# Optimization experiments

Measured on AMD Instinct MI355X. Metric: run time of the kernel, lower is better.

The kernel has to match this reference:

```python
import jax, jax.numpy as jnp
import numpy as np

EPS_BN = 1e-5
EPS_NORM = 1e-12
NUM_HEADS = 8


def _bn_relu(x):
    # BatchNorm2d in training mode with fresh params (gamma=1, beta=0), then ReLU.
    m = x.mean((0, 2, 3), keepdims=True)
    v = x.var((0, 2, 3), keepdims=True)  # biased variance, as PyTorch uses for normalization
    return jax.nn.relu((x - m) * jax.lax.rsqrt(v + EPS_BN))


def _conv3(x, w, groups=1):
    # 3x3 conv, stride 1, padding 1 (NCHW / OIHW)
    return jax.lax.conv_general_dilated(
        x, w, (1, 1), ((1, 1), (1, 1)),
        dimension_numbers=('NCHW', 'OIHW', 'NCHW'),
        feature_group_count=groups)


def _encoder(x, w1, w2, w3):
    # Conv1x1 -> BN -> ReLU -> Conv k2 s2 -> BN -> ReLU -> Conv1x1 -> BN -> ReLU
    x = _bn_relu(jnp.einsum('bihw,oi->bohw', x, w1))
    b, c, h, w = x.shape
    # k=2,s=2 conv as a reshape + einsum (non-overlapping 2x2 patches)
    x = _bn_relu(jnp.einsum('bchpwq,ocpq->bohw', x.reshape(b, c, h // 2, 2, w // 2, 2), w2))
    return _bn_relu(jnp.einsum('bihw,oi->bohw', x, w3))


def _decoder(x, w1, w2, w3):
    # ConvT1x1 -> BN -> ReLU -> ConvT k2 s2 -> BN -> ReLU -> ConvT1x1 -> BN -> ReLU
    x = _bn_relu(jnp.einsum('bihw,io->bohw', x, w1))
    # ConvTranspose k=2,s=2: each input pixel expands to a 2x2 block
    y = jnp.einsum('bihw,iopq->bohpwq', x, w2)
    b, o, h, p, w, q = y.shape
    x = _bn_relu(y.reshape(b, o, h * p, w * q))
    return _bn_relu(jnp.einsum('bihw,io->bohw', x, w3))


def _l2norm(x):
    # F.normalize(dim=-1) with eps=1e-12
    return x / jnp.maximum(jnp.linalg.norm(x, axis=-1, keepdims=True), EPS_NORM)


def setup_inputs() -> dict:
    key = jax.random.key(0)
    ks = jax.random.split(key, 13)
    B, C, H, W = 8, 256, 64, 64
    d = C // 4  # attention dim after self.divide

    def rn(k, shape, s=0.1):
        return jax.random.normal(k, shape, jnp.float32) * s

    return {
        'x': jax.random.normal(ks[0], (B, C, H, W), jnp.float32),
        'y': jax.random.normal(ks[1], (B, C, H, W), jnp.float32),
        'temperature': jnp.ones((NUM_HEADS, 1, 1), jnp.float32),
        'enc_w1': rn(ks[2], (d // 2, C)),
        'enc_w2': rn(ks[3], (d // 2, d // 2, 2, 2)),
        'enc_w3': rn(ks[4], (d, d // 2)),
        'kv_w': rn(ks[5], (2 * d, d)),
        'kv_dw_w': rn(ks[6], (2 * d, 1, 3, 3)),
        'q_w': rn(ks[7], (d, d)),
        'q_dw_w': rn(ks[8], (d, d, 3, 3)),
        'proj_w': rn(ks[9], (d, d)),
        'dec_w1': rn(ks[10], (d, 2 * d)),
        'dec_w2': rn(ks[11], (2 * d, 2 * d, 2, 2)),
        'dec_w3': rn(ks[12], (2 * d, 4 * d)),
    }


def reference(x, y, temperature, enc_w1, enc_w2, enc_w3, kv_w, kv_dw_w,
              q_w, q_dw_w, proj_w, dec_w1, dec_w2, dec_w3):
    # Shared freshly-built encoder applied to both x and y (same weights,
    # BN batch stats computed per call).
    x = _encoder(x, enc_w1, enc_w2, enc_w3)
    y = _encoder(y, enc_w1, enc_w2, enc_w3)
    b, c, h, w = x.shape  # c = 64, h = w = 32

    kv = _conv3(jnp.einsum('bihw,oi->bohw', x, kv_w), kv_dw_w, groups=2 * c)
    k, v = jnp.split(kv, 2, axis=1)
    q = _conv3(jnp.einsum('bihw,oi->bohw', y, q_w), q_dw_w)  # regular 3x3 conv

    ch = c // NUM_HEADS
    heads = lambda t: t.reshape(b, NUM_HEADS, ch, h * w)  # b head c (h w)
    q, k, v = heads(q), heads(k), heads(v)
    q = _l2norm(q)
    k = _l2norm(k)
    temp = temperature[None]  # [1, head, 1, 1]

    # Spatial attention: [b, head, hw, hw]
    attn_s = jax.nn.softmax(jnp.einsum('bhcn,bhcm->bhnm', q, k) * temp, axis=-1)
    out_s = jnp.einsum('bhcn,bhnm->bhcm', v, attn_s).reshape(b, c, h, w)
    out_s = jnp.einsum('bihw,oi->bohw', out_s, proj_w)

    # Channel attention: [b, head, c, c]
    attn_c = jax.nn.softmax(jnp.einsum('bhcn,bhdn->bhcd', q, k) * temp, axis=-1)
    out_c = jnp.einsum('bhcd,bhdn->bhcn', attn_c, v).reshape(b, c, h, w)
    out_c = jnp.einsum('bihw,oi->bohw', out_c, proj_w)

    return _decoder(out_s + out_c, dec_w1, dec_w2, dec_w3)
```

## Files before the change

### kernel.cpp

```cpp
#include <hip/hip_runtime.h>
#include <hip/hip_bf16.h>

#define EPS_BN 1e-5f

#define PIPE_FENCE() asm volatile("" ::: "memory")

template<int OT, bool HASBN, bool HASSTATS>
__global__ __launch_bounds__(256,2) void conv1x1_lds(
    const float* __restrict__ in0, const float* __restrict__ in1,
    const float* __restrict__ w, float* __restrict__ out,
    const float* __restrict__ stIn, float* __restrict__ stOut,
    int I, int O, int P, int wio, int zsplit, float invN)
{
  constexpr int OB = 4*OT;
  __shared__ __align__(16) float wl[8192];
  __shared__ __align__(16) float4 il[2][8][64];
  __shared__ float bnm[256], bnr[256];

  int tid = threadIdx.x;
  int c   = tid & 63;
  int g   = tid >> 6;
  int z = blockIdx.z;
  int t = (z >= zsplit) ? 1 : 0;
  int b = t ? (z - zsplit) : z;
  const float* in = t ? in1 : in0;
  int o0 = blockIdx.y*OB;
  int P4 = P >> 2;

  if(wio){
    for(int idx=tid; idx<I*OB; idx+=256){
      int i = idx/OB, oo = idx - i*OB;
      wl[idx] = w[(size_t)i*O + o0 + oo];
    }
  } else {
    for(int idx=tid; idx<I*OB; idx+=256){
      int oo = idx/I, i = idx - oo*I;
      wl[i*OB + oo] = w[(size_t)(o0+oo)*I + i];
    }
  }
  if(HASBN){
    for(int i=tid; i<I; i+=256){
      float s  = stIn[((size_t)t*I + i)*2];
      float s2 = stIn[((size_t)t*I + i)*2+1];
      float m  = s*invN;
      bnm[i] = m;
      bnr[i] = rsqrtf(s2*invN - m*m + EPS_BN);
    }
  }

  const float4* inb = (const float4*)(in + (size_t)b*I*P) + (size_t)blockIdx.x*64;

  float4 vr0 = inb[(size_t)g*P4 + c];
  float4 vr1 = inb[(size_t)(g+4)*P4 + c];
  il[0][g][c]   = vr0;
  il[0][g+4][c] = vr1;
  __syncthreads();

  float acc[OT][4];
#pragma unroll
  for(int j=0;j<OT;j++){ acc[j][0]=acc[j][1]=acc[j][2]=acc[j][3]=0.f; }

  int nchunk = I >> 3;
  for(int k=0; k<nchunk; ++k){
    int cur = k & 1;
    if(k+1 < nchunk){
      vr0 = inb[(size_t)((k+1)*8+g)*P4 + c];
      vr1 = inb[(size_t)((k+1)*8+g+4)*P4 + c];
    }
    PIPE_FENCE();
#pragma unroll
    for(int ch=0; ch<8; ++ch){
      float4 v = il[cur][ch][c];
      if(HASBN){
        int i = k*8+ch;
        float m = bnm[i], r = bnr[i];
        v.x = fmaxf((v.x-m)*r, 0.f); v.y = fmaxf((v.y-m)*r, 0.f);
        v.z = fmaxf((v.z-m)*r, 0.f); v.w = fmaxf((v.w-m)*r, 0.f);
      }
      const float4* wr4 = (const float4*)&wl[(k*8+ch)*OB + g*OT];
#pragma unroll
      for(int j4=0;j4<OT/4;j4++){
        float4 wq = wr4[j4];
        int j = j4*4;
        acc[j  ][0]=fmaf(wq.x,v.x,acc[j  ][0]); acc[j  ][1]=fmaf(wq.x,v.y,acc[j  ][1]);
        acc[j  ][2]=fmaf(wq.x,v.z,acc[j  ][2]); acc[j  ][3]=fmaf(wq.x,v.w,acc[j  ][3]);
        acc[j+1][0]=fmaf(wq.y,v.x,acc[j+1][0]); acc[j+1][1]=fmaf(wq.y,v.y,acc[j+1][1]);
        acc[j+1][2]=fmaf(wq.y,v.z,acc[j+1][2]); acc[j+1][3]=fmaf(wq.y,v.w,acc[j+1][3]);
        acc[j+2][0]=fmaf(wq.z,v.x,acc[j+2][0]); acc[j+2][1]=fmaf(wq.z,v.y,acc[j+2][1]);
        acc[j+2][2]=fmaf(wq.z,v.z,acc[j+2][2]); acc[j+2][3]=fmaf(wq.z,v.w,acc[j+2][3]);
        acc[j+3][0]=fmaf(wq.w,v.x,acc[j+3][0]); acc[j+3][1]=fmaf(wq.w,v.y,acc[j+3][1]);
        acc[j+3][2]=fmaf(wq.w,v.z,acc[j+3][2]); acc[j+3][3]=fmaf(wq.w,v.w,acc[j+3][3]);
      }
    }
    PIPE_FENCE();
    if(k+1 < nchunk){
      int nxt = cur^1;
      il[nxt][g][c]   = vr0;
      il[nxt][g+4][c] = vr1;
    }
    __syncthreads();
  }

  float4* ob = (float4*)(out + (size_t)z*O*P) + (size_t)blockIdx.x*64 + c;
#pragma unroll
  for(int j=0;j<OT;j++){
    float4 vv = {acc[j][0], acc[j][1], acc[j][2], acc[j][3]};
    ob[(size_t)(o0 + g*OT + j)*P4] = vv;
  }

  if(HASSTATS){
#pragma unroll
    for(int j=0;j<OT;j++){
      float s  = acc[j][0]+acc[j][1]+acc[j][2]+acc[j][3];
      float s2 = acc[j][0]*acc[j][0]+acc[j][1]*acc[j][1]
               + acc[j][2]*acc[j][2]+acc[j][3]*acc[j][3];
      for(int off=32; off>0; off>>=1){
        s  += __shfl_down(s,  off, 64);
        s2 += __shfl_down(s2, off, 64);
      }
      if((tid & 63)==0){
        atomicAdd(&stOut[((size_t)t*O + o0 + g*OT + j)*2],   s);
        atomicAdd(&stOut[((size_t)t*O + o0 + g*OT + j)*2+1], s2);
      }
    }
  }
}

template<int OT, bool HASBN, bool HASSTATS>
__global__ __launch_bounds__(256) void conv1x1_small(
    const float* __restrict__ in0, const float* __restrict__ in1,
    const float* __restrict__ w, float* __restrict__ out,
    const float* __restrict__ stIn, float* __restrict__ stOut,
    int I, int O, int wio, int zsplit, float invN)
{
  __shared__ float wl[512];
  __shared__ float bnm[128], bnr[128];
  int tid = threadIdx.x;
  int z  = blockIdx.z;
  int t  = (z >= zsplit) ? 1 : 0;
  int b  = t ? (z - zsplit) : z;
  const float* in = t ? in1 : in0;
  int W2 = 2*OT;

  for(int idx=tid; idx<I*W2; idx+=256){
    int i = idx/W2, slot = idx - i*W2;
    int oabs = blockIdx.y*W2 + slot;
    wl[idx] = wio ? w[(size_t)i*O + oabs] : w[(size_t)oabs*I + i];
  }
  if(HASBN){
    for(int i=tid; i<I; i+=256){
      float s  = stIn[((size_t)t*I + i)*2];
      float s2 = stIn[((size_t)t*I + i)*2+1];
      float m  = s*invN;
      bnm[i] = m;
      bnr[i] = rsqrtf(s2*invN - m*m + EPS_BN);
    }
  }
  __syncthreads();

  int p4 = blockIdx.x*128 + (tid & 127);
  int os = tid >> 7;
  const float4* inb = (const float4*)(in + (size_t)b*I*1024) + p4;

  float acc[OT][4];
#pragma unroll
  for(int j=0;j<OT;j++){ acc[j][0]=acc[j][1]=acc[j][2]=acc[j][3]=0.f; }

  float4 vb[8];
  for(int i0=0;i0<I;i0+=8){
#pragma unroll
    for(int u=0;u<8;u++) vb[u] = inb[(size_t)(i0+u)*256];
    PIPE_FENCE();
#pragma unroll
    for(int u=0;u<8;u++){
      float4 v = vb[u];
      if(HASBN){
        float m = bnm[i0+u], r = bnr[i0+u];
        v.x = fmaxf((v.x-m)*r, 0.f); v.y = fmaxf((v.y-m)*r, 0.f);
        v.z = fmaxf((v.z-m)*r, 0.f); v.w = fmaxf((v.w-m)*r, 0.f);
      }
      const float* wr = &wl[(i0+u)*W2 + os*OT];
#pragma unroll
      for(int j=0;j<OT;j++){
        float wv = wr[j];
        acc[j][0] = fmaf(wv, v.x, acc[j][0]);
        acc[j][1] = fmaf(wv, v.y, acc[j][1]);
        acc[j][2] = fmaf(wv, v.z, acc[j][2]);
        acc[j][3] = fmaf(wv, v.w, acc[j][3]);
      }
    }
  }

  int obase = blockIdx.y*W2 + os*OT;
  float4* ob = (float4*)(out + ((size_t)z*O + obase)*1024) + p4;
#pragma unroll
  for(int j=0;j<OT;j++){
    float4 vv = {acc[j][0], acc[j][1], acc[j][2], acc[j][3]};
    ob[(size_t)j*256] = vv;
  }

  if(HASSTATS){
#pragma unroll
    for(int j=0;j<OT;j++){
      float s  = acc[j][0]+acc[j][1]+acc[j][2]+acc[j][3];
      float s2 = acc[j][0]*acc[j][0]+acc[j][1]*acc[j][1]
               + acc[j][2]*acc[j][2]+acc[j][3]*acc[j][3];
      for(int off=32; off>0; off>>=1){
        s  += __shfl_down(s,  off, 64);
        s2 += __shfl_down(s2, off, 64);
      }
      if((tid & 63)==0){
        atomicAdd(&stOut[((size_t)t*O + obase + j)*2],   s);
        atomicAdd(&stOut[((size_t)t*O + obase + j)*2+1], s2);
      }
    }
  }
}

__global__ __launch_bounds__(256) void conv2x2s2_bn_kernel(
    const float* __restrict__ in, const float* __restrict__ w,
    float* __restrict__ out, const float* __restrict__ stIn,
    float* __restrict__ stOut, float invN)
{
  __shared__ float wl[512];
  __shared__ float bnm[32], bnr[32];
  int tid = threadIdx.x;
  int o0 = blockIdx.x*4;
  int rq = blockIdx.y;
  int z  = blockIdx.z;
  int t  = z >> 3;

  for(int idx=tid; idx<512; idx+=256){
    int osub = idx>>7, ch=(idx>>2)&31, pq=idx&3;
    wl[idx] = w[(((size_t)(o0+osub)*32 + ch)*4) + pq];
  }
  if(tid < 32){
    float s  = stIn[((size_t)t*32 + tid)*2];
    float s2 = stIn[((size_t)t*32 + tid)*2+1];
    float m  = s*invN;
    bnm[tid] = m;
    bnr[tid] = rsqrtf(s2*invN - m*m + EPS_BN);
  }
  __syncthreads();

  int os   = tid >> 6;
  int slot = tid & 63;
  int h    = rq*8 + (slot>>3);
  int wg   = slot & 7;
  int cb   = wg*8;
  const float* wbase = &wl[os*128];
  const float* inz = in + (size_t)z*32*4096;

  float acc[4] = {0,0,0,0};
  float4 c0,c1,c2,c3, n0_,n1_,n2_,n3_;
  c0 = *(const float4*)(inz + (size_t)0*4096 + (2*h)*64 + cb);
  c1 = *(const float4*)(inz + (size_t)0*4096 + (2*h)*64 + cb + 4);
  c2 = *(const float4*)(inz + (size_t)0*4096 + (2*h+1)*64 + cb);
  c3 = *(const float4*)(inz + (size_t)0*4096 + (2*h+1)*64 + cb + 4);
  for(int ch=0; ch<32; ch++){
    if(ch < 31){
      n0_ = *(const float4*)(inz + (size_t)(ch+1)*4096 + (2*h)*64 + cb);
      n1_ = *(const float4*)(inz + (size_t)(ch+1)*4096 + (2*h)*64 + cb + 4);
      n2_ = *(const float4*)(inz + (size_t)(ch+1)*4096 + (2*h+1)*64 + cb);
      n3_ = *(const float4*)(inz + (size_t)(ch+1)*4096 + (2*h+1)*64 + cb + 4);
    }
    float m = bnm[ch], r = bnr[ch];
    float t0[8] = {c0.x,c0.y,c0.z,c0.w,c1.x,c1.y,c1.z,c1.w};
    float t1[8] = {c2.x,c2.y,c2.z,c2.w,c3.x,c3.y,c3.z,c3.w};
#pragma unroll
    for(int e=0;e<8;e++){
      t0[e] = fmaxf((t0[e]-m)*r, 0.f);
      t1[e] = fmaxf((t1[e]-m)*r, 0.f);
    }
    const float* wp = wbase + ch*4;
#pragma unroll
    for(int k=0;k<4;k++){
      acc[k] = fmaf(wp[0], t0[2*k],   acc[k]);
      acc[k] = fmaf(wp[1], t0[2*k+1], acc[k]);
      acc[k] = fmaf(wp[2], t1[2*k],   acc[k]);
      acc[k] = fmaf(wp[3], t1[2*k+1], acc[k]);
    }
    c0=n0_; c1=n1_; c2=n2_; c3=n3_;
  }

  float4 vv = {acc[0],acc[1],acc[2],acc[3]};
  *(float4*)(out + ((size_t)z*32 + o0+os)*1024 + h*32 + wg*4) = vv;

  float s  = acc[0]+acc[1]+acc[2]+acc[3];
  float s2 = acc[0]*acc[0]+acc[1]*acc[1]+acc[2]*acc[2]+acc[3]*acc[3];
  for(int off=32; off>0; off>>=1){
    s  += __shfl_down(s,  off, 64);
    s2 += __shfl_down(s2, off, 64);
  }
  if((tid & 63)==0){
    atomicAdd(&stOut[((size_t)t*32 + o0 + os)*2],   s);
    atomicAdd(&stOut[((size_t)t*32 + o0 + os)*2+1], s2);
  }
}

__global__ __launch_bounds__(256) void upsample2x2_bn_kernel(
    const float* __restrict__ in, const float* __restrict__ w,
    float* __restrict__ out, const float* __restrict__ stIn,
    float* __restrict__ stOut, float invN)
{
  __shared__ float wl[1024];
  __shared__ float bnm[128], bnr[128];
  int tid = threadIdx.x;
  int o0 = blockIdx.x*2;
  int b  = blockIdx.y;

  for(int idx=tid; idx<1024; idx+=256){
    int pq = idx & 3, r = idx >> 2;
    int i = r >> 1, j = r & 1;
    wl[idx] = w[((size_t)i*128 + o0+j)*4 + pq];
  }
  if(tid < 128){
    float s  = stIn[(size_t)tid*2];
    float s2 = stIn[(size_t)tid*2+1];
    float m  = s*invN;
    bnm[tid] = m;
    bnr[tid] = rsqrtf(s2*invN - m*m + EPS_BN);
  }
  __syncthreads();

  int h  = tid >> 3;
  int wg = tid & 7;
  int w0 = wg*4;

  float acc[2][16];
#pragma unroll
  for(int j=0;j<2;j++) for(int e=0;e<16;e++) acc[j][e]=0.f;

  float4 vb4[8];
  for(int i0=0;i0<128;i0+=8){
#pragma unroll
    for(int u=0;u<8;u++)
      vb4[u] = *(const float4*)(in + (((size_t)b*128+i0+u)*1024) + h*32 + w0);
    PIPE_FENCE();
#pragma unroll
    for(int u=0;u<8;u++){
      int i = i0+u;
      float4 v = vb4[u];
      float m = bnm[i], r = bnr[i];
      float vk[4] = {fmaxf((v.x-m)*r,0.f), fmaxf((v.y-m)*r,0.f),
                     fmaxf((v.z-m)*r,0.f), fmaxf((v.w-m)*r,0.f)};
#pragma unroll
      for(int j=0;j<2;j++){
        const float* wj = &wl[(i*2+j)*4];
#pragma unroll
        for(int pq=0;pq<4;pq++){
#pragma unroll
          for(int k=0;k<4;k++)
            acc[j][pq*4+k] = fmaf(wj[pq], vk[k], acc[j][pq*4+k]);
        }
      }
    }
  }

#pragma unroll
  for(int j=0;j<2;j++){
    float* ob = out + ((size_t)b*128 + o0+j)*4096;
#pragma unroll
    for(int p=0;p<2;p++){
      float4 A = {acc[j][(p*2+0)*4+0], acc[j][(p*2+1)*4+0],
                  acc[j][(p*2+0)*4+1], acc[j][(p*2+1)*4+1]};
      float4 B = {acc[j][(p*2+0)*4+2], acc[j][(p*2+1)*4+2],
                  acc[j][(p*2+0)*4+3], acc[j][(p*2+1)*4+3]};
      *(float4*)(ob + (2*h+p)*64 + 2*w0)     = A;
      *(float4*)(ob + (2*h+p)*64 + 2*w0 + 4) = B;
    }
  }

#pragma unroll
  for(int j=0;j<2;j++){
    float s=0.f, s2=0.f;
#pragma unroll
    for(int e=0;e<16;e++){ s += acc[j][e]; s2 += acc[j][e]*acc[j][e]; }
    for(int off=32; off>0; off>>=1){
      s  += __shfl_down(s,  off, 64);
      s2 += __shfl_down(s2, off, 64);
    }
    if((tid & 63)==0){
      atomicAdd(&stOut[((size_t)(o0+j))*2],   s);
      atomicAdd(&stOut[((size_t)(o0+j))*2+1], s2);
    }
  }
}

__global__ __launch_bounds__(256) void bn_final_kernel(
    float* __restrict__ x, const float* __restrict__ st, float invN)
{
  int idx4 = blockIdx.x*256 + threadIdx.x;
  int c = (idx4 >> 10) & 255;
  float s  = st[(size_t)c*2];
  float s2 = st[(size_t)c*2+1];
  float m  = s*invN;
  float r  = rsqrtf(s2*invN - m*m + EPS_BN);
  float4 v = ((float4*)x)[idx4];
  v.x = fmaxf((v.x-m)*r, 0.f); v.y = fmaxf((v.y-m)*r, 0.f);
  v.z = fmaxf((v.z-m)*r, 0.f); v.w = fmaxf((v.w-m)*r, 0.f);
  ((float4*)x)[idx4] = v;
}

__global__ __launch_bounds__(256) void dwconv3x3_kernel(
    const float* __restrict__ in, const float* __restrict__ w,
    float* __restrict__ out, int C)
{
  int c = blockIdx.x, b = blockIdx.y;
  int tid = threadIdx.x;
  __shared__ float wl[9];
  if(tid < 9) wl[tid] = w[c*9 + tid];
  __syncthreads();
  int h = tid >> 3, x4 = tid & 7;
  int c0 = x4*4;
  const float* base = in + ((size_t)b*C + c)*1024;
  float ax=0.f, ay=0.f, az=0.f, aw=0.f;
#pragma unroll
  for(int dr=0; dr<3; dr++){
    int r = h + dr - 1;
    if((unsigned)r >= 32u) continue;
    const float* row = base + r*32 + c0;
    float4 cc = *(const float4*)row;
    float l  = (x4>0) ? row[-1] : 0.f;
    float rr = (x4<7) ? row[4]  : 0.f;
    float w0=wl[dr*3], w1=wl[dr*3+1], w2=wl[dr*3+2];
    ax = fmaf(w0,l,   fmaf(w1,cc.x, fmaf(w2,cc.y, ax)));
    ay = fmaf(w0,cc.x,fmaf(w1,cc.y, fmaf(w2,cc.z, ay)));
    az = fmaf(w0,cc.y,fmaf(w1,cc.z, fmaf(w2,cc.w, az)));
    aw = fmaf(w0,cc.z,fmaf(w1,cc.w, fmaf(w2,rr,  aw)));
  }
  float4 vv = {ax,ay,az,aw};
  *(float4*)(out + ((size_t)b*C + c)*1024 + h*32 + c0) = vv;
}

__global__ __launch_bounds__(256) void conv3x3_kernel(
    const float* __restrict__ in, const float* __restrict__ w,
    float* __restrict__ out, int IC)
{
  int o = blockIdx.x, b = blockIdx.y;
  int tid = threadIdx.x;
  __shared__ float wl[576];
  for(int t=tid; t<IC*9; t+=256) wl[t] = w[(size_t)o*IC*9 + t];
  __syncthreads();
  int h = tid >> 3, x4 = tid & 7;
  int c0 = x4*4;
  const float* inb = in + (size_t)b*IC*1024;
  float ax=0.f, ay=0.f, az=0.f, aw=0.f;
#pragma unroll 2
  for(int i=0;i<IC;i++){
    const float* base = inb + (size_t)i*1024;
    const float* wp = &wl[i*9];
#pragma unroll
    for(int dr=0; dr<3; dr++){
      int r = h + dr - 1;
      if((unsigned)r >= 32u) continue;
      const float* row = base + r*32 + c0;
      float4 cc = *(const float4*)row;
      float l  = (x4>0) ? row[-1] : 0.f;
      float rr = (x4<7) ? row[4]  : 0.f;
      float w0=wp[dr*3], w1=wp[dr*3+1], w2=wp[dr*3+2];
      ax = fmaf(w0,l,   fmaf(w1,cc.x, fmaf(w2,cc.y, ax)));
      ay = fmaf(w0,cc.x,fmaf(w1,cc.y, fmaf(w2,cc.z, ay)));
      az = fmaf(w0,cc.y,fmaf(w1,cc.z, fmaf(w2,cc.w, az)));
      aw = fmaf(w0,cc.z,fmaf(w1,cc.w, fmaf(w2,rr,  aw)));
    }
  }
  float4 vv = {ax,ay,az,aw};
  *(float4*)(out + ((size_t)b*gridDim.x + o)*1024 + h*32 + c0) = vv;
}

__global__ __launch_bounds__(256) void norm_scale_kernel(
    const float* __restrict__ q, const float* __restrict__ kv,
    float* __restrict__ scl)
{
  int r = blockIdx.x;
  const float* p;
  if(r < 512){ int b=r>>6, c=r&63; p = q + ((size_t)b*64+c)*1024; }
  else { int rr=r-512; int b=rr>>6, c=rr&63; p = kv + ((size_t)b*128+c)*1024; }
  int tid = threadIdx.x;
  float4 v = ((const float4*)p)[tid];
  float s = v.x*v.x + v.y*v.y + v.z*v.z + v.w*v.w;
  __shared__ float ls[256];
  ls[tid]=s; __syncthreads();
  for(int st=128; st>0; st>>=1){ if(tid<st) ls[tid]+=ls[tid+st]; __syncthreads(); }
  if(tid==0) scl[r] = 1.f/fmaxf(sqrtf(ls[0]), 1e-12f);
}

__global__ __launch_bounds__(256) void attn_pass1(
    const float* __restrict__ q, const float* __restrict__ kv,
    const float* __restrict__ temp, const float* __restrict__ scl,
    float* __restrict__ den_out)
{
  int bx = blockIdx.x, hh = blockIdx.y, b = blockIdx.z;
  int nchunk = bx >> 2, mq = bx & 3;
  int tid = threadIdx.x;
  __shared__ __align__(16) float kl[256*12];
  const float* kb = kv + ((size_t)b*128 + hh*8)*1024 + mq*256;
  for(int t=tid;t<2048;t+=256){
    int c=t>>8, m=t&255;
    kl[m*12+c] = kb[(size_t)c*1024+m] * scl[512 + b*64 + hh*8 + c];
  }
  __syncthreads();
  int n = nchunk*256 + tid;
  const float* qp = q + ((size_t)b*64 + hh*8)*1024 + n;
  float th = temp[hh];
  float mxb = fabsf(th);
  float qr[8];
#pragma unroll
  for(int c=0;c<8;c++) qr[c] = qp[(size_t)c*1024] * scl[b*64+hh*8+c] * th;
  const float4* kl4 = (const float4*)kl;
  float den = 0.f, den2 = 0.f;
  for(int m=0;m<256;m+=2){
    float4 a  = kl4[m*3],     a2 = kl4[m*3+1];
    float4 bt = kl4[(m+1)*3], b2 = kl4[(m+1)*3+1];
    float s0 = qr[0]*a.x+qr[1]*a.y+qr[2]*a.z+qr[3]*a.w
             + qr[4]*a2.x+qr[5]*a2.y+qr[6]*a2.z+qr[7]*a2.w;
    float s1 = qr[0]*bt.x+qr[1]*bt.y+qr[2]*bt.z+qr[3]*bt.w
             + qr[4]*b2.x+qr[5]*b2.y+qr[6]*b2.z+qr[7]*b2.w;
    den  += __expf(s0 - mxb);
    den2 += __expf(s1 - mxb);
  }
  atomicAdd(&den_out[((size_t)(b*8+hh))*1024+n], den+den2);
}

__global__ __launch_bounds__(256) void attn_pass2(
    const float* __restrict__ q, const float* __restrict__ kv,
    const float* __restrict__ temp, const float* __restrict__ scl,
    const float* __restrict__ den, float* __restrict__ out)
{
  int bx = blockIdx.x, hh = blockIdx.y, b = blockIdx.z;
  int mchunk = bx >> 2, nq = bx & 3;
  int tid = threadIdx.x;
  __shared__ __align__(16) float ql[256*12];
  __shared__ __align__(16) float vl[256*12];
  __shared__ float idl[256];
  int bh = b*8+hh;
  int n0 = nq*256;
  const float* qb = q  + ((size_t)b*64 + hh*8)*1024 + n0;
  const float* vb = kv + ((size_t)b*128 + 64 + hh*8)*1024 + n0;
  for(int t=tid;t<2048;t+=256){
    int c=t>>8, n=t&255;
    ql[n*12+c] = qb[(size_t)c*1024+n] * scl[b*64+hh*8+c];
    vl[n*12+c] = vb[(size_t)c*1024+n];
  }
  idl[tid] = 1.f/den[(size_t)bh*1024 + n0 + tid];
  __syncthreads();
  int m = mchunk*256 + tid;
  const float* kb = kv + ((size_t)b*128 + hh*8)*1024 + m;
  float th = temp[hh];
  float mxb = fabsf(th);
  float kr[8];
#pragma unroll
  for(int c=0;c<8;c++) kr[c] = kb[(size_t)c*1024] * scl[512+b*64+hh*8+c] * th;
  float acc[8] = {0,0,0,0,0,0,0,0};
  const float4* ql4 = (const float4*)ql;
  const float4* vl4 = (const float4*)vl;
  for(int n=0;n<256;n+=2){
    float4 qa = ql4[n*3],     qa2 = ql4[n*3+1];
    float4 qc = ql4[(n+1)*3], qc2 = ql4[(n+1)*3+1];
    float s0 = kr[0]*qa.x+kr[1]*qa.y+kr[2]*qa.z+kr[3]*qa.w
             + kr[4]*qa2.x+kr[5]*qa2.y+kr[6]*qa2.z+kr[7]*qa2.w;
    float s1 = kr[0]*qc.x+kr[1]*qc.y+kr[2]*qc.z+kr[3]*qc.w
             + kr[4]*qc2.x+kr[5]*qc2.y+kr[6]*qc2.z+kr[7]*qc2.w;
    float p0 = __expf(s0 - mxb) * idl[n];
    float p1 = __expf(s1 - mxb) * idl[n+1];
    float4 va = vl4[n*3],     va2 = vl4[n*3+1];
    float4 vc = vl4[(n+1)*3], vc2 = vl4[(n+1)*3+1];
    acc[0]+=p0*va.x + p1*vc.x; acc[1]+=p0*va.y + p1*vc.y;
    acc[2]+=p0*va.z + p1*vc.z; acc[3]+=p0*va.w + p1*vc.w;
    acc[4]+=p0*va2.x + p1*vc2.x; acc[5]+=p0*va2.y + p1*vc2.y;
    acc[6]+=p0*va2.z + p1*vc2.z; acc[7]+=p0*va2.w + p1*vc2.w;
  }
  float* ob = out + ((size_t)b*64 + hh*8)*1024 + m;
#pragma unroll
  for(int c=0;c<8;c++) atomicAdd(&ob[(size_t)c*1024], acc[c]);
}

__global__ __launch_bounds__(256) void attn_channel(
    const float* __restrict__ q, const float* __restrict__ kv,
    const float* __restrict__ temp, const float* __restrict__ scl,
    float* out)
{
  int hh = blockIdx.x, b = blockIdx.y;
  __shared__ float kl[8192];
  const float* qb = q  + ((size_t)b*64 + hh*8)*1024;
  const float* kb = kv + ((size_t)b*128 + hh*8)*1024;
  const float* vb = kv + ((size_t)b*128 + 64 + hh*8)*1024;
  int tid = threadIdx.x;
  for(int t=tid;t<8192;t+=256) kl[t]=kb[t];
  __syncthreads();
  __shared__ float part[256];
  __shared__ float a[64];
  {
    int pair = tid >> 2, seg = tid & 3;
    int c = pair >> 3, d = pair & 7;
    const float* qrow = qb + (size_t)c*1024 + seg*256;
    const float* krow = kl + d*1024 + seg*256;
    float s = 0.f;
#pragma unroll 4
    for(int n=0;n<256;n++) s += qrow[n]*krow[n];
    part[tid] = s;
  }
  __syncthreads();
  if(tid < 64){
    int c = tid >> 3, d = tid & 7;
    float g = part[tid*4]+part[tid*4+1]+part[tid*4+2]+part[tid*4+3];
    part[tid] = g * scl[b*64+hh*8+c] * scl[512+b*64+hh*8+d] * temp[hh];
  }
  __syncthreads();
  if(tid < 8){
    float mx = -3.4e38f;
    for(int d=0;d<8;d++) mx = fmaxf(mx, part[tid*8+d]);
    float den = 0.f;
    float e[8];
    for(int d=0;d<8;d++){ e[d] = __expf(part[tid*8+d]-mx); den+=e[d]; }
    float inv = 1.f/den;
    for(int d=0;d<8;d++) a[tid*8+d] = e[d]*inv;
  }
  __syncthreads();
  float* ob = out + ((size_t)b*64 + hh*8)*1024;
  for(int n=tid;n<1024;n+=256){
    float vv[8];
#pragma unroll
    for(int d=0;d<8;d++) vv[d] = vb[(size_t)d*1024+n];
#pragma unroll
    for(int c=0;c<8;c++){
      float s = 0.f;
#pragma unroll
      for(int d=0;d<8;d++) s += a[c*8+d]*vv[d];
      ob[(size_t)c*1024+n] += s;
    }
  }
}

extern "C" void kernel_launch(void* const* d_in, const int* in_sizes, int n_in,
                              void* d_out, int out_size, void* d_ws, size_t ws_size,
                              hipStream_t stream)
{
  (void)in_sizes; (void)n_in; (void)out_size; (void)ws_size;
  const float* x      = (const float*)d_in[0];
  const float* y      = (const float*)d_in[1];
  const float* temp   = (const float*)d_in[2];
  const float* enc_w1 = (const float*)d_in[3];
  const float* enc_w2 = (const float*)d_in[4];
  const float* enc_w3 = (const float*)d_in[5];
  const float* kv_w   = (const float*)d_in[6];
  const float* kv_dw_w= (const float*)d_in[7];
  const float* q_w    = (const float*)d_in[8];
  const float* q_dw_w = (const float*)d_in[9];
  const float* proj_w = (const float*)d_in[10];
  const float* dec_w1 = (const float*)d_in[11];
  const float* dec_w2 = (const float*)d_in[12];
  const float* dec_w3 = (const float*)d_in[13];
  float* out = (float*)d_out;

  float* W   = (float*)d_ws;
  float* ST  = W;
  float* ST0 = ST;
  float* ST1 = ST + 128;
  float* ST2 = ST + 256;
  float* ST3 = ST + 512;
  float* ST4 = ST + 768;
  float* ST5 = ST + 1024;
  float* A    = W + 2048;
  float* E1   = A;
  float* KV1  = A;
  float* QPre = A + 1048576;
  float* ATTN = A;
  float* PROJ = A + 524288;
  float* D1   = A + 1048576;
  float* E2   = W + 2099200;
  float* E3   = W + 2623488;
  float* KV   = W + 3672064;
  float* Q    = W + 4720640;
  float* SCL  = W + 5244928;
  float* DEN  = W + 5245952;
  float* D2   = W + 2099200;

  const float inv32k = 1.f/32768.f, inv8k = 1.f/8192.f;

  hipMemsetAsync(ST, 0, 2048*sizeof(float), stream);
  hipMemsetAsync(DEN, 0, 65536*sizeof(float), stream);

  conv1x1_lds<8,false,true><<<dim3(16,1,16),256,0,stream>>>(
      x, y, enc_w1, E1, nullptr, ST0, 256, 32, 4096, 0, 8, 0.f);
  conv2x2s2_bn_kernel<<<dim3(8,4,16),256,0,stream>>>(E1, enc_w2, E2, ST0, ST1, inv32k);
  conv1x1_small<4,true,true><<<dim3(2,8,16),256,0,stream>>>(
      E2, E2 + (size_t)8*32*1024, enc_w3, E3, ST1, ST2, 32, 64, 0, 8, inv8k);

  conv1x1_small<4,true,false><<<dim3(2,16,8),256,0,stream>>>(
      E3, E3, kv_w, KV1, ST2, nullptr, 64, 128, 0, 999, inv8k);
  dwconv3x3_kernel<<<dim3(128,8),256,0,stream>>>(KV1, kv_dw_w, KV, 128);
  conv1x1_small<4,true,false><<<dim3(2,8,8),256,0,stream>>>(
      E3 + (size_t)8*64*1024, E3, q_w, QPre, ST2 + 128, nullptr, 64, 64, 0, 999, inv8k);
  conv3x3_kernel<<<dim3(64,8),256,0,stream>>>(QPre, q_dw_w, Q, 64);

  hipMemsetAsync(ATTN, 0, 524288*sizeof(float), stream);

  norm_scale_kernel<<<1024,256,0,stream>>>(Q, KV, SCL);

  attn_pass1<<<dim3(16,8,8),256,0,stream>>>(Q, KV, temp, SCL, DEN);
  attn_pass2<<<dim3(16,8,8),256,0,stream>>>(Q, KV, temp, SCL, DEN, ATTN);
  attn_channel<<<dim3(8,8),256,0,stream>>>(Q, KV, temp, SCL, ATTN);

  conv1x1_small<4,false,false><<<dim3(2,8,8),256,0,stream>>>(
      ATTN, ATTN, proj_w, PROJ, nullptr, nullptr, 64, 64, 0, 999, 0.f);

  conv1x1_small<4,false,true><<<dim3(2,16,8),256,0,stream>>>(
      PROJ, PROJ, dec_w1, D1, nullptr, ST3, 64, 128, 1, 999, 0.f);
  upsample2x2_bn_kernel<<<dim3(64,8),256,0,stream>>>(D1, dec_w2, D2, ST3, ST4, inv8k);
  conv1x1_lds<16,true,true><<<dim3(16,4,8),256,0,stream>>>(
      D2, D2, dec_w3, out, ST4, ST5, 128, 256, 4096, 1, 999, inv32k);
  bn_final_kernel<<<8192,256,0,stream>>>(out, ST5, inv32k);
}
```

Before: 610.9 us.

## Replace LDS-staged 1x1 conv with wave-shuffle input sharing and retune small convs

Rewrites the large 1x1 conv kernel so each wavefront loads its own input columns into registers and shares them across output groups with cross-lane shuffles. This drops the shared-memory input double buffer and its per-chunk block barriers. The kernel now has a configurable output-group count, and the stats reduction runs over sub-wave widths. Separately, the small 1x1 conv launches go from 4 to 1 outputs per thread with more blocks, trading per-thread reuse for parallelism.

Result: slower. 956.3 us (+56.5%).

```diff
diff --git a/kernel.cpp b/kernel.cpp
--- a/kernel.cpp
+++ b/kernel.cpp
@@ -5,21 +5,25 @@
 
 #define PIPE_FENCE() asm volatile("" ::: "memory")
 
-template<int OT, bool HASBN, bool HASSTATS>
-__global__ __launch_bounds__(256,2) void conv1x1_lds(
+template<int OG, int OT, bool HASBN, bool HASSTATS>
+__global__ __launch_bounds__(256) void conv1x1_shfl(
     const float* __restrict__ in0, const float* __restrict__ in1,
     const float* __restrict__ w, float* __restrict__ out,
     const float* __restrict__ stIn, float* __restrict__ stOut,
     int I, int O, int P, int wio, int zsplit, float invN)
 {
-  constexpr int OB = 4*OT;
-  __shared__ __align__(16) float wl[8192];
-  __shared__ __align__(16) float4 il[2][8][64];
+  constexpr int OB  = OG*OT;
+  constexpr int CW  = 64/OG;
+  constexpr int OBq = OB/4;
+  constexpr int OTq = OT/4;
+  __shared__ float wl[8192];
   __shared__ float bnm[256], bnr[256];
 
-  int tid = threadIdx.x;
-  int c   = tid & 63;
-  int g   = tid >> 6;
+  int tid  = threadIdx.x;
+  int lane = tid & 63;
+  int wid  = tid >> 6;
+  int c    = lane & (CW-1);
+  int g    = lane / CW;
   int z = blockIdx.z;
   int t = (z >= zsplit) ? 1 : 0;
   int b = t ? (z - zsplit) : z;
@@ -47,61 +51,56 @@
       bnr[i] = rsqrtf(s2*invN - m*m + EPS_BN);
     }
   }
-
-  const float4* inb = (const float4*)(in + (size_t)b*I*P) + (size_t)blockIdx.x*64;
-
-  float4 vr0 = inb[(size_t)g*P4 + c];
-  float4 vr1 = inb[(size_t)(g+4)*P4 + c];
-  il[0][g][c]   = vr0;
-  il[0][g+4][c] = vr1;
-  __syncthreads();
+  __syncthreads();
+
+  int colbase = (blockIdx.x*4 + wid)*CW;
+  const float4* inb = (const float4*)(in + (size_t)b*I*P) + colbase + c;
+  const float4* wl4 = (const float4*)wl;
 
   float acc[OT][4];
 #pragma unroll
   for(int j=0;j<OT;j++){ acc[j][0]=acc[j][1]=acc[j][2]=acc[j][3]=0.f; }
 
-  int nchunk = I >> 3;
-  for(int k=0; k<nchunk; ++k){
-    int cur = k & 1;
-    if(k+1 < nchunk){
-      vr0 = inb[(size_t)((k+1)*8+g)*P4 + c];
-      vr1 = inb[(size_t)((k+1)*8+g+4)*P4 + c];
-    }
+  float4 vr[4];
+  for(int i0=0; i0<I; i0+=4*OG){
+#pragma unroll
+    for(int u=0;u<4;u++) vr[u] = inb[(size_t)(i0 + g + u*OG)*P4];
     PIPE_FENCE();
 #pragma unroll
-    for(int ch=0; ch<8; ++ch){
-      float4 v = il[cur][ch][c];
-      if(HASBN){
-        int i = k*8+ch;
-        float m = bnm[i], r = bnr[i];
-        v.x = fmaxf((v.x-m)*r, 0.f); v.y = fmaxf((v.y-m)*r, 0.f);
-        v.z = fmaxf((v.z-m)*r, 0.f); v.w = fmaxf((v.w-m)*r, 0.f);
+    for(int u=0;u<4;u++){
+#pragma unroll
+      for(int gs=0; gs<OG; gs++){
+        int i = i0 + u*OG + gs;
+        int src = gs*CW + c;
+        float4 v;
+        v.x = __shfl(vr[u].x, src);
+        v.y = __shfl(vr[u].y, src);
+        v.z = __shfl(vr[u].z, src);
+        v.w = __shfl(vr[u].w, src);
+        if(HASBN){
+          float m = bnm[i], r = bnr[i];
+          v.x = fmaxf((v.x-m)*r, 0.f); v.y = fmaxf((v.y-m)*r, 0.f);
+          v.z = fmaxf((v.z-m)*r, 0.f); v.w = fmaxf((v.w-m)*r, 0.f);
+        }
+        const float4* wr4 = &wl4[(size_t)i*OBq + g*OTq];
+#pragma unroll
+        for(int j4=0;j4<OTq;j4++){
+          float4 wq = wr4[j4];
+          int j = j4*4;
+          acc[j  ][0]=fmaf(wq.x,v.x,acc[j  ][0]); acc[j  ][1]=fmaf(wq.x,v.y,acc[j  ][1]);
+          acc[j  ][2]=fmaf(wq.x,v.z,acc[j  ][2]); acc[j  ][3]=fmaf(wq.x,v.w,acc[j  ][3]);
+          acc[j+1][0]=fmaf(wq.y,v.x,acc[j+1][0]); acc[j+1][1]=fmaf(wq.y,v.y,acc[j+1][1]);
+          acc[j+1][2]=fmaf(wq.y,v.z,acc[j+1][2]); acc[j+1][3]=fmaf(wq.y,v.w,acc[j+1][3]);
+          acc[j+2][0]=fmaf(wq.z,v.x,acc[j+2][0]); acc[j+2][1]=fmaf(wq.z,v.y,acc[j+2][1]);
+          acc[j+2][2]=fmaf(wq.z,v.z,acc[j+2][2]); acc[j+2][3]=fmaf(wq.z,v.w,acc[j+2][3]);
+          acc[j+3][0]=fmaf(wq.w,v.x,acc[j+3][0]); acc[j+3][1]=fmaf(wq.w,v.y,acc[j+3][1]);
+          acc[j+3][2]=fmaf(wq.w,v.z,acc[j+3][2]); acc[j+3][3]=fmaf(wq.w,v.w,acc[j+3][3]);
+        }
       }
-      const float4* wr4 = (const float4*)&wl[(k*8+ch)*OB + g*OT];
-#pragma unroll
-      for(int j4=0;j4<OT/4;j4++){
-        float4 wq = wr4[j4];
-        int j = j4*4;
-        acc[j  ][0]=fmaf(wq.x,v.x,acc[j  ][0]); acc[j  ][1]=fmaf(wq.x,v.y,acc[j  ][1]);
-        acc[j  ][2]=fmaf(wq.x,v.z,acc[j  ][2]); acc[j  ][3]=fmaf(wq.x,v.w,acc[j  ][3]);
-        acc[j+1][0]=fmaf(wq.y,v.x,acc[j+1][0]); acc[j+1][1]=fmaf(wq.y,v.y,acc[j+1][1]);
-        acc[j+1][2]=fmaf(wq.y,v.z,acc[j+1][2]); acc[j+1][3]=fmaf(wq.y,v.w,acc[j+1][3]);
-        acc[j+2][0]=fmaf(wq.z,v.x,acc[j+2][0]); acc[j+2][1]=fmaf(wq.z,v.y,acc[j+2][1]);
-        acc[j+2][2]=fmaf(wq.z,v.z,acc[j+2][2]); acc[j+2][3]=fmaf(wq.z,v.w,acc[j+2][3]);
-        acc[j+3][0]=fmaf(wq.w,v.x,acc[j+3][0]); acc[j+3][1]=fmaf(wq.w,v.y,acc[j+3][1]);
-        acc[j+3][2]=fmaf(wq.w,v.z,acc[j+3][2]); acc[j+3][3]=fmaf(wq.w,v.w,acc[j+3][3]);
-      }
-    }
-    PIPE_FENCE();
-    if(k+1 < nchunk){
-      int nxt = cur^1;
-      il[nxt][g][c]   = vr0;
-      il[nxt][g+4][c] = vr1;
-    }
-    __syncthreads();
-  }
-
-  float4* ob = (float4*)(out + (size_t)z*O*P) + (size_t)blockIdx.x*64 + c;
+    }
+  }
+
+  float4* ob = (float4*)(out + (size_t)z*O*P) + colbase + c;
 #pragma unroll
   for(int j=0;j<OT;j++){
     float4 vv = {acc[j][0], acc[j][1], acc[j][2], acc[j][3]};
@@ -114,11 +113,12 @@
       float s  = acc[j][0]+acc[j][1]+acc[j][2]+acc[j][3];
       float s2 = acc[j][0]*acc[j][0]+acc[j][1]*acc[j][1]
                + acc[j][2]*acc[j][2]+acc[j][3]*acc[j][3];
-      for(int off=32; off>0; off>>=1){
-        s  += __shfl_down(s,  off, 64);
-        s2 += __shfl_down(s2, off, 64);
+#pragma unroll
+      for(int off=CW/2; off>0; off>>=1){
+        s  += __shfl_down(s,  off, CW);
+        s2 += __shfl_down(s2, off, CW);
       }
-      if((tid & 63)==0){
+      if(c==0){
         atomicAdd(&stOut[((size_t)t*O + o0 + g*OT + j)*2],   s);
         atomicAdd(&stOut[((size_t)t*O + o0 + g*OT + j)*2+1], s2);
       }
@@ -682,16 +682,16 @@
   hipMemsetAsync(ST, 0, 2048*sizeof(float), stream);
   hipMemsetAsync(DEN, 0, 65536*sizeof(float), stream);
 
-  conv1x1_lds<8,false,true><<<dim3(16,1,16),256,0,stream>>>(
+  conv1x1_shfl<8,4,false,true><<<dim3(32,1,16),256,0,stream>>>(
       x, y, enc_w1, E1, nullptr, ST0, 256, 32, 4096, 0, 8, 0.f);
   conv2x2s2_bn_kernel<<<dim3(8,4,16),256,0,stream>>>(E1, enc_w2, E2, ST0, ST1, inv32k);
-  conv1x1_small<4,true,true><<<dim3(2,8,16),256,0,stream>>>(
+  conv1x1_small<1,true,true><<<dim3(2,32,16),256,0,stream>>>(
       E2, E2 + (size_t)8*32*1024, enc_w3, E3, ST1, ST2, 32, 64, 0, 8, inv8k);
 
-  conv1x1_small<4,true,false><<<dim3(2,16,8),256,0,stream>>>(
+  conv1x1_small<1,true,false><<<dim3(2,64,8),256,0,stream>>>(
       E3, E3, kv_w, KV1, ST2, nullptr, 64, 128, 0, 999, inv8k);
   dwconv3x3_kernel<<<dim3(128,8),256,0,stream>>>(KV1, kv_dw_w, KV, 128);
-  conv1x1_small<4,true,false><<<dim3(2,8,8),256,0,stream>>>(
+  conv1x1_small<1,true,false><<<dim3(2,32,8),256,0,stream>>>(
       E3 + (size_t)8*64*1024, E3, q_w, QPre, ST2 + 128, nullptr, 64, 64, 0, 999, inv8k);
   conv3x3_kernel<<<dim3(64,8),256,0,stream>>>(QPre, q_dw_w, Q, 64);
 
@@ -703,13 +703,13 @@
   attn_pass2<<<dim3(16,8,8),256,0,stream>>>(Q, KV, temp, SCL, DEN, ATTN);
   attn_channel<<<dim3(8,8),256,0,stream>>>(Q, KV, temp, SCL, ATTN);
 
-  conv1x1_small<4,false,false><<<dim3(2,8,8),256,0,stream>>>(
+  conv1x1_small<1,false,false><<<dim3(2,32,8),256,0,stream>>>(
       ATTN, ATTN, proj_w, PROJ, nullptr, nullptr, 64, 64, 0, 999, 0.f);
 
-  conv1x1_small<4,false,true><<<dim3(2,16,8),256,0,stream>>>(
+  conv1x1_small<1,false,true><<<dim3(2,64,8),256,0,stream>>>(
       PROJ, PROJ, dec_w1, D1, nullptr, ST3, 64, 128, 1, 999, 0.f);
   upsample2x2_bn_kernel<<<dim3(64,8),256,0,stream>>>(D1, dec_w2, D2, ST3, ST4, inv8k);
-  conv1x1_lds<16,true,true><<<dim3(16,4,8),256,0,stream>>>(
+  conv1x1_shfl<4,16,true,true><<<dim3(16,4,8),256,0,stream>>>(
       D2, D2, dec_w3, out, ST4, ST5, 128, 256, 4096, 1, 999, inv32k);
   bn_final_kernel<<<8192,256,0,stream>>>(out, ST5, inv32k);
 }
```
